# Kernel tuning notes

Hardware: AMD Instinct MI355X
Metric: run time of the kernel (lower is better)

## Reference

```python
import jax, jax.numpy as jnp
import numpy as np

B, N, C, H = 1, 128, 128, 8
D = C // H
SCALE = D ** -0.5


def layer_norm(x, w, b, eps=1e-5):
    m = jnp.mean(x, axis=-1, keepdims=True)
    v = jnp.var(x, axis=-1, keepdims=True)
    return (x - m) * jax.lax.rsqrt(v + eps) * w + b


def setup_inputs() -> dict:
    key = jax.random.key(0)
    ks = jax.random.split(key, 8)
    s = 0.02
    return {
        "e": jax.random.normal(ks[0], (B, N, N, C), jnp.float32),
        "mask": jnp.zeros((B, N, N, 1), jnp.float32),
        "ln_w": jnp.ones((C,), jnp.float32),
        "ln_b": jnp.zeros((C,), jnp.float32),
        "w_qkv_in": jax.random.normal(ks[1], (C, 3 * C), jnp.float32) * s,
        "b_qkv_in": jnp.zeros((3 * C,), jnp.float32),
        "w_eg_in": jax.random.normal(ks[2], (C, 2 * H), jnp.float32) * s,
        "b_eg_in": jnp.zeros((2 * H,), jnp.float32),
        "w_qkv_out": jax.random.normal(ks[3], (C, 3 * C), jnp.float32) * s,
        "b_qkv_out": jnp.zeros((3 * C,), jnp.float32),
        "w_eg_out": jax.random.normal(ks[4], (C, 2 * H), jnp.float32) * s,
        "b_eg_out": jnp.zeros((2 * H,), jnp.float32),
        "w_o": jax.random.normal(ks[5], (2 * C, C), jnp.float32) * s,
        "b_o": jnp.zeros((C,), jnp.float32),
    }


def reference(e, mask, ln_w, ln_b, w_qkv_in, b_qkv_in, w_eg_in, b_eg_in,
              w_qkv_out, b_qkv_out, w_eg_out, b_eg_out, w_o, b_o):
    b, n = e.shape[0], e.shape[1]
    e_ln = layer_norm(e, ln_w, ln_b)

    # ---- incoming-edge stream ----
    qkv = e_ln @ w_qkv_in + b_qkv_in                      # [b,n,n,3C]
    Q, K, V = jnp.split(qkv, 3, axis=-1)
    Q = Q.reshape(b, n, n, D, H) * SCALE                  # bijdh
    K = K.reshape(b, n, n, D, H)
    V = V.reshape(b, n, n, D, H)
    eg = e_ln @ w_eg_in + b_eg_in                         # [b,n,n,2H]
    E_in = eg[..., :H][:, :, None, :, :]                  # [b,i,1,k,h]
    G_in = eg[..., H:][:, :, None, :, :]
    H_in = jnp.einsum('bijdh,bjkdh->bijkh', Q, K) + E_in
    mask_in = mask[:, :, None, :, :]                      # [b,i,1,k,1]
    gates_in = jax.nn.sigmoid(G_in + mask_in)
    A_in = jax.nn.softmax(H_in + mask_in, axis=3) * gates_in
    Va_in = jnp.einsum('bijkh,bjkdh->bijdh', A_in, V)

    # ---- outgoing-edge stream ----
    qkv = e_ln @ w_qkv_out + b_qkv_out
    Q, K, V = jnp.split(qkv, 3, axis=-1)
    Q = Q.reshape(b, n, n, D, H) * SCALE
    K = K.reshape(b, n, n, D, H)
    V = V.reshape(b, n, n, D, H)
    eg = e_ln @ w_eg_out + b_eg_out
    E_out = eg[..., :H][:, :, :, None, :]                 # [b,k,i,1,h]
    G_out = eg[..., H:][:, :, :, None, :]
    H_out = jnp.einsum('bijdh,bkjdh->bkijh', Q, K) + E_out
    mask_out = mask[:, :, :, None, :]                     # [b,k,i,1,1]
    gates_out = jax.nn.sigmoid(G_out + mask_out)
    A_out = jax.nn.softmax(H_out + mask_out, axis=1) * gates_out
    Va_out = jnp.einsum('bkijh,bkjdh->bijdh', A_out, V)

    Va = jnp.concatenate([Va_in, Va_out], axis=-1).reshape(b, n, n, 2 * C)
    return Va @ w_o + b_o
```

## Files before the change

### kernel.cpp

```cpp
#include <hip/hip_runtime.h>
#include <hip/hip_bf16.h>


#define NPOS 16384
#define CDIM 128

typedef __attribute__((ext_vector_type(8))) short bf16x8;
typedef __attribute__((ext_vector_type(8))) unsigned short u16x8;
typedef __attribute__((ext_vector_type(4))) float f32x4;

#define MFMA16(a, b, c) __builtin_amdgcn_mfma_f32_16x16x32_bf16((a), (b), (c), 0, 0, 0)

#define GLL16(gp, lp) __builtin_amdgcn_global_load_lds( \
    (const __attribute__((address_space(1))) void*)(gp), \
    (__attribute__((address_space(3))) void*)(lp), 16, 0, 0)

static __device__ __forceinline__ unsigned short f2bf(float x) {
    union { float f; unsigned int u; } v; v.f = x;
    unsigned int u = v.u;
    unsigned int r = u + 0x7FFFu + ((u >> 16) & 1u);
    return (unsigned short)(r >> 16);
}
static __device__ __forceinline__ float bf2f(unsigned short h) {
    union { float f; unsigned int u; } v; v.u = ((unsigned int)h) << 16; return v.f;
}

__global__ __launch_bounds__(256) void prep_kernel(
    const float* __restrict__ e, const float* __restrict__ lnw,
    const float* __restrict__ lnb, unsigned short* __restrict__ e_hl,
    const float* __restrict__ wq1, const float* __restrict__ we1,
    unsigned short* __restrict__ B1t,
    const float* __restrict__ wq2, const float* __restrict__ we2,
    unsigned short* __restrict__ B2t,
    const float* __restrict__ wo, unsigned short* __restrict__ B3t)
{
    const int t = threadIdx.x;
    const int bx = blockIdx.x;
    if (bx < 4096) {
        const int lane = t & 63;
        const int row = bx * 4 + (t >> 6);
        float2 x = *(const float2*)(e + (size_t)row * CDIM + lane * 2);
        float s = x.x + x.y, s2 = x.x * x.x + x.y * x.y;
        #pragma unroll
        for (int off = 1; off < 64; off <<= 1) {
            s  += __shfl_xor(s,  off, 64);
            s2 += __shfl_xor(s2, off, 64);
        }
        float m = s * (1.f / 128.f);
        float v = s2 * (1.f / 128.f) - m * m;
        float sc = rsqrtf(v + 1e-5f);
        float2 wv = *(const float2*)(lnw + lane * 2);
        float2 bv = *(const float2*)(lnb + lane * 2);
        float y0 = (x.x - m) * sc * wv.x + bv.x;
        float y1 = (x.y - m) * sc * wv.y + bv.y;
        unsigned short h0 = f2bf(y0), h1 = f2bf(y1);
        ushort2 hi = {h0, h1};
        ushort2 lo = {f2bf(y0 - bf2f(h0)), f2bf(y1 - bf2f(h1))};
        *(ushort2*)(e_hl + (size_t)row * 256 + lane * 2)       = hi;
        *(ushort2*)(e_hl + (size_t)row * 256 + 128 + lane * 2) = lo;
    } else if (bx < 4544) {
        int pb = bx - 4096;
        const float* wq; const float* we; unsigned short* Bt;
        if (pb < 224) { wq = wq1; we = we1; Bt = B1t; }
        else          { pb -= 224; wq = wq2; we = we2; Bt = B2t; }
        const int idx = pb * 256 + t;
        const int n = idx >> 7, k = idx & 127;
        float v = 0.f;
        if (n < 384) v = wq[(size_t)k * 384 + n];
        else if (n < 400) v = we[(size_t)k * 16 + (n - 384)];
        unsigned short hi = f2bf(v);
        Bt[idx] = hi;
        Bt[448 * 128 + idx] = f2bf(v - bf2f(hi));
    } else {
        const int idx = (bx - 4544) * 256 + t;
        const int n = idx >> 8, kp = idx & 255;
        const int d = kp & 15, pl = kp >> 4;
        const int k = d * 16 + pl;
        float v = wo[(size_t)k * 128 + n];
        unsigned short hi = f2bf(v);
        B3t[idx] = hi;
        B3t[128 * 256 + idx] = f2bf(v - bf2f(hi));
    }
}

__global__ __launch_bounds__(256) void gemm_qkv_kernel(
    const unsigned short* __restrict__ e_hl,
    const unsigned short* __restrict__ B1t, const unsigned short* __restrict__ B2t,
    const float* __restrict__ bq_i, const float* __restrict__ be_i,
    const float* __restrict__ bq_o, const float* __restrict__ be_o,
    const float* __restrict__ mask,
    unsigned short* __restrict__ QT, unsigned short* __restrict__ KT,
    unsigned short* __restrict__ VT,
    unsigned short* __restrict__ Etab, unsigned short* __restrict__ Gtab)
{
    __shared__ __align__(16) unsigned char smem[24576];
    unsigned short* Alds = (unsigned short*)smem;
    unsigned short* Blds = (unsigned short*)(smem + 16384);

    const int t = threadIdx.x;
    const int wave = t >> 6, lane = t & 63;
    const int m = lane & 15, q = lane >> 4;
    const int c = blockIdx.x;
    const int bx = ((c & 31) << 2) | (c >> 5);
    const int W0blk = bx * 128;
    const int by = blockIdx.y;
    const int N0 = by * 64;
    const int br = blockIdx.z;
    const unsigned short* Bt = br ? B2t : B1t;
    const float* bias_qkv = br ? bq_o : bq_i;
    const float* bias_eg  = br ? be_o : be_i;

    f32x4 acc[2][4];
    #pragma unroll
    for (int a = 0; a < 2; ++a)
        #pragma unroll
        for (int cc = 0; cc < 4; ++cc) acc[a][cc] = (f32x4){0.f, 0.f, 0.f, 0.f};

    for (int kc = 0; kc < 4; ++kc) {
        #pragma unroll
        for (int ii = 0; ii < 6; ++ii) {
            const int id = wave + ii * 4;
            if (id < 16) {
                const int hl = id >> 3, s = id & 7;
                const int qq = s >> 1, rbase = (s & 1) * 64;
                const unsigned short* g = e_hl
                    + (size_t)(W0blk + rbase + lane) * 256 + hl * 128 + kc * 32 + qq * 8;
                unsigned short* l = Alds + hl * 4096 + qq * 1024 + rbase * 8;
                GLL16(g, l);
            } else {
                const int id2 = id - 16;
                const int hl = id2 >> 2, qq = id2 & 3;
                const unsigned short* g = Bt + (size_t)(N0 + lane) * 128
                    + hl * (448 * 128) + kc * 32 + qq * 8;
                unsigned short* l = Blds + hl * 2048 + qq * 512;
                GLL16(g, l);
            }
        }
        __syncthreads();

        bf16x8 aH[2], aL[2], bH[4], bL[4];
        #pragma unroll
        for (int ms = 0; ms < 2; ++ms) {
            const int row = wave * 32 + ms * 16 + m;
            aH[ms] = *(const bf16x8*)(Alds + 0    + q * 1024 + row * 8);
            aL[ms] = *(const bf16x8*)(Alds + 4096 + q * 1024 + row * 8);
        }
        #pragma unroll
        for (int ns = 0; ns < 4; ++ns) {
            bH[ns] = *(const bf16x8*)(Blds + 0    + q * 512 + (ns * 16 + m) * 8);
            bL[ns] = *(const bf16x8*)(Blds + 2048 + q * 512 + (ns * 16 + m) * 8);
        }
        #pragma unroll
        for (int ns = 0; ns < 4; ++ns) {
            acc[0][ns] = MFMA16(aH[0], bH[ns], acc[0][ns]);
            acc[1][ns] = MFMA16(aH[1], bH[ns], acc[1][ns]);
        }
        #pragma unroll
        for (int ns = 0; ns < 4; ++ns) {
            acc[0][ns] = MFMA16(aL[0], bH[ns], acc[0][ns]);
            acc[1][ns] = MFMA16(aL[1], bH[ns], acc[1][ns]);
        }
        #pragma unroll
        for (int ns = 0; ns < 4; ++ns) {
            acc[0][ns] = MFMA16(aH[0], bL[ns], acc[0][ns]);
            acc[1][ns] = MFMA16(aH[1], bL[ns], acc[1][ns]);
        }
        __syncthreads();
    }

    if (by < 6) {
        unsigned short (*Ts16)[66] = (unsigned short (*)[66])smem;
        #pragma unroll
        for (int ms = 0; ms < 2; ++ms)
            #pragma unroll
            for (int ns = 0; ns < 4; ++ns) {
                const int lc = ns * 16 + m;
                const int col = N0 + lc;
                const float bias = bias_qkv[col];
                const float scale = (col < 128) ? 0.25f : 1.f;
                #pragma unroll
                for (int r = 0; r < 4; ++r) {
                    const int lr = wave * 32 + ms * 16 + q * 4 + r;
                    Ts16[lr][lc] = f2bf((acc[ms][ns][r] + bias) * scale);
                }
            }
        __syncthreads();
        const int qsel = by >> 1, dhalf = by & 1;
        unsigned short* dstH = (qsel == 0) ? QT : (qsel == 1 ? KT : VT);
        const bool tr = (qsel == 0) || (br == 1);
        #pragma unroll
        for (int it = 0; it < 4; ++it) {
            int item = it * 256 + t;
            int hh = item >> 7, lr = item & 127;
            u16x8 hi;
            #pragma unroll
            for (int dd = 0; dd < 8; ++dd)
                hi[dd] = Ts16[lr][dd * 8 + hh];
            const size_t sub = ((size_t)(br * 8 + hh) * 2 + dhalf) * NPOS;
            const size_t p16 = tr ? ((size_t)lr * 128 + bx)
                                  : ((size_t)bx * 128 + lr);
            *(u16x8*)(dstH + (sub + p16) * 8) = hi;
        }
    } else {
        float* Tf = (float*)smem;
        #pragma unroll
        for (int ms = 0; ms < 2; ++ms) {
            const float bias = bias_eg[m];
            #pragma unroll
            for (int r = 0; r < 4; ++r) {
                const int lr = wave * 32 + ms * 16 + q * 4 + r;
                Tf[lr * 33 + m] = acc[ms][0][r] + bias;
            }
        }
        __syncthreads();
        const int r128 = t & 127, grp = t >> 7;
        const float mk = mask[bx * 128 + r128];
        const int dst = br ? (r128 * 128 + bx) : (bx * 128 + r128);
        if (grp == 0) {
            #pragma unroll
            for (int h = 0; h < 8; ++h)
                Etab[(size_t)(br * 8 + h) * NPOS + dst] =
                    f2bf(Tf[r128 * 33 + h] + mk);
        } else {
            #pragma unroll
            for (int h = 0; h < 8; ++h) {
                const float g = Tf[r128 * 33 + 8 + h] + mk;
                Gtab[(size_t)(br * 8 + h) * NPOS + dst] =
                    f2bf(1.f / (1.f + __expf(-g)));
            }
        }
    }
}

__global__ __launch_bounds__(256) void attn_kernel(
    const unsigned short* __restrict__ QT, const unsigned short* __restrict__ KT,
    const unsigned short* __restrict__ VT,
    const unsigned short* __restrict__ Etab, const unsigned short* __restrict__ Gtab,
    unsigned short* __restrict__ vaH, unsigned short* __restrict__ vaL)
{
    const int bid = blockIdx.x;
    const int plane = bid >> 6;
    const int j0 = (bid & 63) * 2;
    const int t = threadIdx.x;
    const int wave = t >> 6, lane = t & 63;
    const int m = lane & 15, q = lane >> 4;
    const size_t SP = (size_t)NPOS * 8;
    const unsigned short* __restrict__ Eb = Etab + (size_t)plane * NPOS;
    const unsigned short* __restrict__ Gb = Gtab + (size_t)plane * NPOS;

    __shared__ unsigned short Vth[16 * 136];
    __shared__ unsigned short Pl[128 * 136];

    const int strip = wave * 32;

    u16x8 Ec[2][4], Gc[2][4];
    #pragma unroll
    for (int mt = 0; mt < 2; ++mt)
        #pragma unroll
        for (int r = 0; r < 4; ++r) {
            const int i = strip + mt * 16 + q * 4 + r;
            Ec[mt][r] = *(const u16x8*)(Eb + (size_t)i * 128 + m * 8);
            Gc[mt][r] = *(const u16x8*)(Gb + (size_t)i * 128 + m * 8);
        }

    for (int it = 0; it < 2; ++it) {
        const int j = j0 + it;
        const size_t jb = (size_t)j * 128 * 8;

        f32x4 S[2][8];
        #pragma unroll
        for (int mt = 0; mt < 2; ++mt)
            #pragma unroll
            for (int r = 0; r < 4; ++r) {
                #pragma unroll
                for (int nt = 0; nt < 8; ++nt)
                    S[mt][nt][r] = bf2f(Ec[mt][r][nt]);
            }

        {
            int c = t >> 1, ch = t & 1;
            int krow = (c & 15) * 8 + (c >> 4);
            const unsigned short* src = VT + (size_t)(plane * 2 + ch) * SP + jb
                                      + (size_t)krow * 8;
            u16x8 v = *(const u16x8*)src;
            #pragma unroll
            for (int dd = 0; dd < 8; ++dd)
                Vth[(ch * 8 + dd) * 136 + c] = v[dd];
        }

        const bf16x8 zero8 = {};
        const int hf = q & 1;
        const size_t qko = (size_t)(plane * 2 + hf) * SP + jb;

        bf16x8 aQ[2];
        #pragma unroll
        for (int mt = 0; mt < 2; ++mt) {
            const size_t off = qko + (size_t)(strip + mt * 16 + m) * 8;
            aQ[mt] = (q < 2) ? *(const bf16x8*)(QT + off) : zero8;
        }

        #pragma unroll
        for (int nt = 0; nt < 8; ++nt) {
            const size_t koff = qko + (size_t)(m * 8 + nt) * 8;
            bf16x8 bK = (q < 2) ? *(const bf16x8*)(KT + koff) : zero8;
            #pragma unroll
            for (int mt = 0; mt < 2; ++mt)
                S[mt][nt] = MFMA16(aQ[mt], bK, S[mt][nt]);
        }

        #pragma unroll
        for (int mt = 0; mt < 2; ++mt)
            #pragma unroll
            for (int r = 0; r < 4; ++r) {
                float v = -1e30f;
                #pragma unroll
                for (int nt = 0; nt < 8; ++nt) v = fmaxf(v, S[mt][nt][r]);
                v = fmaxf(v, __shfl_xor(v, 1)); v = fmaxf(v, __shfl_xor(v, 2));
                v = fmaxf(v, __shfl_xor(v, 4)); v = fmaxf(v, __shfl_xor(v, 8));
                float s = 0.f;
                #pragma unroll
                for (int nt = 0; nt < 8; ++nt) {
                    float p = __expf(S[mt][nt][r] - v);
                    S[mt][nt][r] = p;
                    s += p;
                }
                s += __shfl_xor(s, 1); s += __shfl_xor(s, 2);
                s += __shfl_xor(s, 4); s += __shfl_xor(s, 8);
                const float inv = 1.f / s;
                const int i = strip + mt * 16 + q * 4 + r;
                #pragma unroll
                for (int nt = 0; nt < 4; ++nt) {
                    Pl[i * 136 + nt * 16 + m] =
                        f2bf(S[mt][nt][r] * inv * bf2f(Gc[mt][r][nt]));
                    Pl[i * 136 + (nt + 4) * 16 + m] =
                        f2bf(S[mt][nt + 4][r] * inv * bf2f(Gc[mt][r][nt + 4]));
                }
            }

        __syncthreads();

        f32x4 av[2] = {(f32x4){0.f, 0.f, 0.f, 0.f}, (f32x4){0.f, 0.f, 0.f, 0.f}};
        #pragma unroll
        for (int kc = 0; kc < 4; ++kc) {
            const int off = kc * 32 + q * 8;
            bf16x8 bV = *(const bf16x8*)&Vth[m * 136 + off];
            #pragma unroll
            for (int mt = 0; mt < 2; ++mt) {
                bf16x8 aP = *(const bf16x8*)&Pl[(strip + mt * 16 + m) * 136 + off];
                av[mt] = MFMA16(aP, bV, av[mt]);
            }
        }

        #pragma unroll
        for (int mt = 0; mt < 2; ++mt)
            #pragma unroll
            for (int r = 0; r < 4; ++r) {
                const int i = strip + mt * 16 + q * 4 + r;
                const size_t addr = ((size_t)(j * 128 + i)) * 256 + plane * 16 + m;
                const float x = av[mt][r];
                const unsigned short hi = f2bf(x);
                vaH[addr] = hi;
                vaL[addr] = f2bf(x - bf2f(hi));
            }
        __syncthreads();
    }
}

__global__ __launch_bounds__(256) void gemm_out_kernel(
    const unsigned short* __restrict__ vaH,
    const unsigned short* __restrict__ vaL,
    const unsigned short* __restrict__ B3t,
    const float* __restrict__ bias,
    float* __restrict__ out)
{
    const int t = threadIdx.x;
    const int wave = t >> 6, lane = t & 63;
    const int m = lane & 15, q = lane >> 4;
    const int W0 = (blockIdx.x >> 1) * 64 + wave * 16;
    const int N0 = (blockIdx.x & 1) * 64;

    f32x4 acc[4];
    #pragma unroll
    for (int cc = 0; cc < 4; ++cc) acc[cc] = (f32x4){0.f, 0.f, 0.f, 0.f};

    const unsigned short* arowH = vaH + (size_t)(W0 + m) * 256;
    const unsigned short* arowL = vaL + (size_t)(W0 + m) * 256;
    const unsigned short* bcol[4];
    #pragma unroll
    for (int ns = 0; ns < 4; ++ns)
        bcol[ns] = B3t + (size_t)(N0 + ns * 16 + m) * 256;

    #pragma unroll 2
    for (int kc = 0; kc < 8; ++kc) {
        const int ko = kc * 32 + q * 8;
        bf16x8 ah = *(const bf16x8*)(arowH + ko);
        bf16x8 al = *(const bf16x8*)(arowL + ko);
        bf16x8 bh[4], bl[4];
        #pragma unroll
        for (int ns = 0; ns < 4; ++ns) {
            bh[ns] = *(const bf16x8*)(bcol[ns] + ko);
            bl[ns] = *(const bf16x8*)(bcol[ns] + 128 * 256 + ko);
        }
        #pragma unroll
        for (int ns = 0; ns < 4; ++ns) acc[ns] = MFMA16(ah, bh[ns], acc[ns]);
        #pragma unroll
        for (int ns = 0; ns < 4; ++ns) acc[ns] = MFMA16(al, bh[ns], acc[ns]);
        #pragma unroll
        for (int ns = 0; ns < 4; ++ns) acc[ns] = MFMA16(ah, bl[ns], acc[ns]);
    }

    #pragma unroll
    for (int ns = 0; ns < 4; ++ns) {
        const int col = N0 + ns * 16 + m;
        #pragma unroll
        for (int r = 0; r < 4; ++r) {
            const int prow = W0 + q * 4 + r;
            const int orow = ((prow & 127) << 7) | (prow >> 7);
            out[(size_t)orow * 128 + col] = acc[ns][r] + bias[col];
        }
    }
}

extern "C" void kernel_launch(void* const* d_in, const int* in_sizes, int n_in,
                              void* d_out, int out_size, void* d_ws, size_t ws_size,
                              hipStream_t stream) {
    const float* e        = (const float*)d_in[0];
    const float* mask     = (const float*)d_in[1];
    const float* ln_w     = (const float*)d_in[2];
    const float* ln_b     = (const float*)d_in[3];
    const float* w_qkv_in = (const float*)d_in[4];
    const float* b_qkv_in = (const float*)d_in[5];
    const float* w_eg_in  = (const float*)d_in[6];
    const float* b_eg_in  = (const float*)d_in[7];
    const float* w_qkv_o  = (const float*)d_in[8];
    const float* b_qkv_o  = (const float*)d_in[9];
    const float* w_eg_o   = (const float*)d_in[10];
    const float* b_eg_o   = (const float*)d_in[11];
    const float* w_o      = (const float*)d_in[12];
    const float* b_o      = (const float*)d_in[13];
    float* out = (float*)d_out;

    char* base = (char*)d_ws;
    const size_t PLANE = (size_t)16 * NPOS * 16;
    unsigned short* e_hl = (unsigned short*)base;
    unsigned short* QT = (unsigned short*)(base + (size_t)NPOS * 256 * 2);
    unsigned short* KT = QT + PLANE;
    unsigned short* VT = KT + PLANE;
    unsigned short* vaH = VT + PLANE;
    unsigned short* vaL = vaH + (size_t)NPOS * 256;
    unsigned short* Etab = vaL + (size_t)NPOS * 256;
    unsigned short* Gtab = Etab + (size_t)16 * NPOS;
    unsigned short* B3t  = Gtab + (size_t)16 * NPOS;

    unsigned short* B1t = vaH;
    unsigned short* B2t = B1t + (size_t)2 * 448 * 128;

    prep_kernel<<<4672, 256, 0, stream>>>(
        e, ln_w, ln_b, e_hl,
        w_qkv_in, w_eg_in, B1t, w_qkv_o, w_eg_o, B2t, w_o, B3t);

    gemm_qkv_kernel<<<dim3(128, 7, 2), 256, 0, stream>>>(
        e_hl, B1t, B2t, b_qkv_in, b_eg_in, b_qkv_o, b_eg_o, mask,
        QT, KT, VT, Etab, Gtab);

    attn_kernel<<<1024, 256, 0, stream>>>(
        QT, KT, VT, Etab, Gtab, vaH, vaL);

    gemm_out_kernel<<<512, 256, 0, stream>>>(vaH, vaL, B3t, b_o, out);
}
```

Baseline: 185.7 us.

## Split attention to one j per block and pack hi/lo Va into one buffer

The attention kernel now launches one block per (j, head, branch) instead of looping over two j values per block. E/G are loaded per use instead of cached in registers, the V load is issued early, and a min-blocks-per-CU launch bound is added to raise occupancy. The bf16 hi/lo split of Va is packed into a single 32-bit interleaved buffer, so each store and the gemm_out load is one wider access instead of two. In exchange, E/G reuse across the two j iterations is lost and the grid doubles in size.

```diff
diff --git a/kernel.cpp b/kernel.cpp
--- a/kernel.cpp
+++ b/kernel.cpp
@@ -7,6 +7,7 @@
 
 typedef __attribute__((ext_vector_type(8))) short bf16x8;
 typedef __attribute__((ext_vector_type(8))) unsigned short u16x8;
+typedef __attribute__((ext_vector_type(8))) unsigned int u32x8;
 typedef __attribute__((ext_vector_type(4))) float f32x4;
 
 #define MFMA16(a, b, c) __builtin_amdgcn_mfma_f32_16x16x32_bf16((a), (b), (c), 0, 0, 0)
@@ -232,19 +233,19 @@
     }
 }
 
-__global__ __launch_bounds__(256) void attn_kernel(
+__global__ __launch_bounds__(256, 4) void attn_kernel(
     const unsigned short* __restrict__ QT, const unsigned short* __restrict__ KT,
     const unsigned short* __restrict__ VT,
     const unsigned short* __restrict__ Etab, const unsigned short* __restrict__ Gtab,
-    unsigned short* __restrict__ vaH, unsigned short* __restrict__ vaL)
+    unsigned int* __restrict__ vaP)
 {
-    const int bid = blockIdx.x;
-    const int plane = bid >> 6;
-    const int j0 = (bid & 63) * 2;
+    const int j = blockIdx.x, h = blockIdx.y, br = blockIdx.z;
     const int t = threadIdx.x;
     const int wave = t >> 6, lane = t & 63;
     const int m = lane & 15, q = lane >> 4;
+    const int plane = br * 8 + h;
     const size_t SP = (size_t)NPOS * 8;
+    const size_t jb = (size_t)j * 128 * 8;
     const unsigned short* __restrict__ Eb = Etab + (size_t)plane * NPOS;
     const unsigned short* __restrict__ Gb = Gtab + (size_t)plane * NPOS;
 
@@ -253,122 +254,105 @@
 
     const int strip = wave * 32;
 
-    u16x8 Ec[2][4], Gc[2][4];
+    const int vc = t >> 1, vch = t & 1;
+    const int vkrow = (vc & 15) * 8 + (vc >> 4);
+    const u16x8 vv = *(const u16x8*)(VT + (size_t)(plane * 2 + vch) * SP + jb
+                                     + (size_t)vkrow * 8);
+
+    f32x4 S[2][8];
     #pragma unroll
     for (int mt = 0; mt < 2; ++mt)
         #pragma unroll
         for (int r = 0; r < 4; ++r) {
             const int i = strip + mt * 16 + q * 4 + r;
-            Ec[mt][r] = *(const u16x8*)(Eb + (size_t)i * 128 + m * 8);
-            Gc[mt][r] = *(const u16x8*)(Gb + (size_t)i * 128 + m * 8);
-        }
-
-    for (int it = 0; it < 2; ++it) {
-        const int j = j0 + it;
-        const size_t jb = (size_t)j * 128 * 8;
-
-        f32x4 S[2][8];
+            u16x8 ev = *(const u16x8*)(Eb + (size_t)i * 128 + m * 8);
+            #pragma unroll
+            for (int nt = 0; nt < 8; ++nt) S[mt][nt][r] = bf2f(ev[nt]);
+        }
+
+    const bf16x8 zero8 = {};
+    const int hf = q & 1;
+    const size_t qko = (size_t)(plane * 2 + hf) * SP + jb;
+
+    bf16x8 aQ[2];
+    #pragma unroll
+    for (int mt = 0; mt < 2; ++mt) {
+        const size_t off = qko + (size_t)(strip + mt * 16 + m) * 8;
+        aQ[mt] = (q < 2) ? *(const bf16x8*)(QT + off) : zero8;
+    }
+
+    #pragma unroll
+    for (int nt = 0; nt < 8; ++nt) {
+        const size_t koff = qko + (size_t)(m * 8 + nt) * 8;
+        bf16x8 bK = (q < 2) ? *(const bf16x8*)(KT + koff) : zero8;
         #pragma unroll
         for (int mt = 0; mt < 2; ++mt)
-            #pragma unroll
-            for (int r = 0; r < 4; ++r) {
-                #pragma unroll
-                for (int nt = 0; nt < 8; ++nt)
-                    S[mt][nt][r] = bf2f(Ec[mt][r][nt]);
-            }
-
-        {
-            int c = t >> 1, ch = t & 1;
-            int krow = (c & 15) * 8 + (c >> 4);
-            const unsigned short* src = VT + (size_t)(plane * 2 + ch) * SP + jb
-                                      + (size_t)krow * 8;
-            u16x8 v = *(const u16x8*)src;
-            #pragma unroll
-            for (int dd = 0; dd < 8; ++dd)
-                Vth[(ch * 8 + dd) * 136 + c] = v[dd];
-        }
-
-        const bf16x8 zero8 = {};
-        const int hf = q & 1;
-        const size_t qko = (size_t)(plane * 2 + hf) * SP + jb;
-
-        bf16x8 aQ[2];
+            S[mt][nt] = MFMA16(aQ[mt], bK, S[mt][nt]);
+    }
+
+    #pragma unroll
+    for (int mt = 0; mt < 2; ++mt)
+        #pragma unroll
+        for (int r = 0; r < 4; ++r) {
+            float v = -1e30f;
+            #pragma unroll
+            for (int nt = 0; nt < 8; ++nt) v = fmaxf(v, S[mt][nt][r]);
+            v = fmaxf(v, __shfl_xor(v, 1)); v = fmaxf(v, __shfl_xor(v, 2));
+            v = fmaxf(v, __shfl_xor(v, 4)); v = fmaxf(v, __shfl_xor(v, 8));
+            float s = 0.f;
+            #pragma unroll
+            for (int nt = 0; nt < 8; ++nt) {
+                float p = __expf(S[mt][nt][r] - v);
+                S[mt][nt][r] = p;
+                s += p;
+            }
+            s += __shfl_xor(s, 1); s += __shfl_xor(s, 2);
+            s += __shfl_xor(s, 4); s += __shfl_xor(s, 8);
+            const float inv = 1.f / s;
+            const int i = strip + mt * 16 + q * 4 + r;
+            u16x8 gv = *(const u16x8*)(Gb + (size_t)i * 128 + m * 8);
+            #pragma unroll
+            for (int nt = 0; nt < 4; ++nt) {
+                Pl[i * 136 + nt * 16 + m] =
+                    f2bf(S[mt][nt][r] * inv * bf2f(gv[nt]));
+                Pl[i * 136 + (nt + 4) * 16 + m] =
+                    f2bf(S[mt][nt + 4][r] * inv * bf2f(gv[nt + 4]));
+            }
+        }
+
+    #pragma unroll
+    for (int dd = 0; dd < 8; ++dd)
+        Vth[(vch * 8 + dd) * 136 + vc] = vv[dd];
+
+    __syncthreads();
+
+    f32x4 av[2] = {(f32x4){0.f, 0.f, 0.f, 0.f}, (f32x4){0.f, 0.f, 0.f, 0.f}};
+    #pragma unroll
+    for (int kc = 0; kc < 4; ++kc) {
+        const int off = kc * 32 + q * 8;
+        bf16x8 bV = *(const bf16x8*)&Vth[m * 136 + off];
         #pragma unroll
         for (int mt = 0; mt < 2; ++mt) {
-            const size_t off = qko + (size_t)(strip + mt * 16 + m) * 8;
-            aQ[mt] = (q < 2) ? *(const bf16x8*)(QT + off) : zero8;
-        }
-
-        #pragma unroll
-        for (int nt = 0; nt < 8; ++nt) {
-            const size_t koff = qko + (size_t)(m * 8 + nt) * 8;
-            bf16x8 bK = (q < 2) ? *(const bf16x8*)(KT + koff) : zero8;
-            #pragma unroll
-            for (int mt = 0; mt < 2; ++mt)
-                S[mt][nt] = MFMA16(aQ[mt], bK, S[mt][nt]);
-        }
-
-        #pragma unroll
-        for (int mt = 0; mt < 2; ++mt)
-            #pragma unroll
-            for (int r = 0; r < 4; ++r) {
-                float v = -1e30f;
-                #pragma unroll
-                for (int nt = 0; nt < 8; ++nt) v = fmaxf(v, S[mt][nt][r]);
-                v = fmaxf(v, __shfl_xor(v, 1)); v = fmaxf(v, __shfl_xor(v, 2));
-                v = fmaxf(v, __shfl_xor(v, 4)); v = fmaxf(v, __shfl_xor(v, 8));
-                float s = 0.f;
-                #pragma unroll
-                for (int nt = 0; nt < 8; ++nt) {
-                    float p = __expf(S[mt][nt][r] - v);
-                    S[mt][nt][r] = p;
-                    s += p;
-                }
-                s += __shfl_xor(s, 1); s += __shfl_xor(s, 2);
-                s += __shfl_xor(s, 4); s += __shfl_xor(s, 8);
-                const float inv = 1.f / s;
-                const int i = strip + mt * 16 + q * 4 + r;
-                #pragma unroll
-                for (int nt = 0; nt < 4; ++nt) {
-                    Pl[i * 136 + nt * 16 + m] =
-                        f2bf(S[mt][nt][r] * inv * bf2f(Gc[mt][r][nt]));
-                    Pl[i * 136 + (nt + 4) * 16 + m] =
-                        f2bf(S[mt][nt + 4][r] * inv * bf2f(Gc[mt][r][nt + 4]));
-                }
-            }
-
-        __syncthreads();
-
-        f32x4 av[2] = {(f32x4){0.f, 0.f, 0.f, 0.f}, (f32x4){0.f, 0.f, 0.f, 0.f}};
-        #pragma unroll
-        for (int kc = 0; kc < 4; ++kc) {
-            const int off = kc * 32 + q * 8;
-            bf16x8 bV = *(const bf16x8*)&Vth[m * 136 + off];
-            #pragma unroll
-            for (int mt = 0; mt < 2; ++mt) {
-                bf16x8 aP = *(const bf16x8*)&Pl[(strip + mt * 16 + m) * 136 + off];
-                av[mt] = MFMA16(aP, bV, av[mt]);
-            }
-        }
-
-        #pragma unroll
-        for (int mt = 0; mt < 2; ++mt)
-            #pragma unroll
-            for (int r = 0; r < 4; ++r) {
-                const int i = strip + mt * 16 + q * 4 + r;
-                const size_t addr = ((size_t)(j * 128 + i)) * 256 + plane * 16 + m;
-                const float x = av[mt][r];
-                const unsigned short hi = f2bf(x);
-                vaH[addr] = hi;
-                vaL[addr] = f2bf(x - bf2f(hi));
-            }
-        __syncthreads();
-    }
+            bf16x8 aP = *(const bf16x8*)&Pl[(strip + mt * 16 + m) * 136 + off];
+            av[mt] = MFMA16(aP, bV, av[mt]);
+        }
+    }
+
+    #pragma unroll
+    for (int mt = 0; mt < 2; ++mt)
+        #pragma unroll
+        for (int r = 0; r < 4; ++r) {
+            const int i = strip + mt * 16 + q * 4 + r;
+            const size_t addr = ((size_t)(j * 128 + i)) * 256 + plane * 16 + m;
+            const float x = av[mt][r];
+            const unsigned short hi = f2bf(x);
+            const unsigned short lo = f2bf(x - bf2f(hi));
+            vaP[addr] = (unsigned int)hi | ((unsigned int)lo << 16);
+        }
 }
 
 __global__ __launch_bounds__(256) void gemm_out_kernel(
-    const unsigned short* __restrict__ vaH,
-    const unsigned short* __restrict__ vaL,
+    const unsigned int* __restrict__ vaP,
     const unsigned short* __restrict__ B3t,
     const float* __restrict__ bias,
     float* __restrict__ out)
@@ -383,8 +367,7 @@
     #pragma unroll
     for (int cc = 0; cc < 4; ++cc) acc[cc] = (f32x4){0.f, 0.f, 0.f, 0.f};
 
-    const unsigned short* arowH = vaH + (size_t)(W0 + m) * 256;
-    const unsigned short* arowL = vaL + (size_t)(W0 + m) * 256;
+    const unsigned int* arow = vaP + (size_t)(W0 + m) * 256;
     const unsigned short* bcol[4];
     #pragma unroll
     for (int ns = 0; ns < 4; ++ns)
@@ -393,8 +376,13 @@
     #pragma unroll 2
     for (int kc = 0; kc < 8; ++kc) {
         const int ko = kc * 32 + q * 8;
-        bf16x8 ah = *(const bf16x8*)(arowH + ko);
-        bf16x8 al = *(const bf16x8*)(arowL + ko);
+        u32x8 w = *(const u32x8*)(arow + ko);
+        bf16x8 ah, al;
+        #pragma unroll
+        for (int jj = 0; jj < 8; ++jj) {
+            ah[jj] = (short)(w[jj] & 0xffffu);
+            al[jj] = (short)(w[jj] >> 16);
+        }
         bf16x8 bh[4], bl[4];
         #pragma unroll
         for (int ns = 0; ns < 4; ++ns) {
@@ -446,13 +434,12 @@
     unsigned short* QT = (unsigned short*)(base + (size_t)NPOS * 256 * 2);
     unsigned short* KT = QT + PLANE;
     unsigned short* VT = KT + PLANE;
-    unsigned short* vaH = VT + PLANE;
-    unsigned short* vaL = vaH + (size_t)NPOS * 256;
-    unsigned short* Etab = vaL + (size_t)NPOS * 256;
+    unsigned int* vaP = (unsigned int*)(VT + PLANE);
+    unsigned short* Etab = (unsigned short*)(vaP + (size_t)NPOS * 256);
     unsigned short* Gtab = Etab + (size_t)16 * NPOS;
     unsigned short* B3t  = Gtab + (size_t)16 * NPOS;
 
-    unsigned short* B1t = vaH;
+    unsigned short* B1t = (unsigned short*)vaP;
     unsigned short* B2t = B1t + (size_t)2 * 448 * 128;
 
     prep_kernel<<<4672, 256, 0, stream>>>(
@@ -463,8 +450,8 @@
         e_hl, B1t, B2t, b_qkv_in, b_eg_in, b_qkv_o, b_eg_o, mask,
         QT, KT, VT, Etab, Gtab);
 
-    attn_kernel<<<1024, 256, 0, stream>>>(
-        QT, KT, VT, Etab, Gtab, vaH, vaL);
-
-    gemm_out_kernel<<<512, 256, 0, stream>>>(vaH, vaL, B3t, b_o, out);
-}
+    attn_kernel<<<dim3(128, 8, 2), 256, 0, stream>>>(
+        QT, KT, VT, Etab, Gtab, vaP);
+
+    gemm_out_kernel<<<512, 256, 0, stream>>>(vaP, B3t, b_o, out);
+}
```

After: 161.8 us. 1.15x faster.
